# Kernel tuning notes

Hardware: AMD Instinct MI355X
Metric: run time of the kernel (lower is better)

## Reference

```python
import jax, jax.numpy as jnp
import numpy as np

NU, NBU, NI, D, L = 50000, 20000, 100000, 64, 2
C_TEMP = 0.25


def setup_inputs() -> dict:
    key = jax.random.key(0)
    ks = jax.random.split(key, 11)
    B, E_ui, E_ub, E_bi = 2048, 1_500_000, 1_000_000, 1_000_000
    return {
        "users": jax.random.randint(ks[0], (B,), 0, NU, dtype=jnp.int32),
        "bundles": jax.random.randint(ks[1], (B, 2), 0, NBU, dtype=jnp.int32),
        "ui_u": jax.random.randint(ks[2], (E_ui,), 0, NU, dtype=jnp.int32),
        "ui_i": jax.random.randint(ks[3], (E_ui,), 0, NI, dtype=jnp.int32),
        "ub_u": jax.random.randint(ks[4], (E_ub,), 0, NU, dtype=jnp.int32),
        "ub_b": jax.random.randint(ks[5], (E_ub,), 0, NBU, dtype=jnp.int32),
        "bi_b": jax.random.randint(ks[6], (E_bi,), 0, NBU, dtype=jnp.int32),
        "bi_i": jax.random.randint(ks[7], (E_bi,), 0, NI, dtype=jnp.int32),
        "users_feature": jax.random.normal(ks[8], (NU, D), jnp.float32) * 0.1,
        "bundles_feature": jax.random.normal(ks[9], (NBU, D), jnp.float32) * 0.1,
        "items_feature": jax.random.normal(ks[10], (NI, D), jnp.float32) * 0.1,
    }


def _sym_norm_vals(rows, cols, n):
    # laplace_transform: D_r^{-1/2} A D_c^{-1/2}; graph is symmetric so row/col degrees coincide
    deg = jax.ops.segment_sum(jnp.ones(rows.shape, jnp.float32), rows, num_segments=n)
    dinv = 1.0 / (jnp.sqrt(deg) + 1e-8)
    return dinv[rows] * dinv[cols]


def _spmm(rows, cols, vals, feat, n):
    return jax.ops.segment_sum(vals[:, None] * feat[cols], rows, num_segments=n)


def _one_propagate(rows, cols, n, A, Bf):
    vals = _sym_norm_vals(rows, cols, n)
    f = jnp.concatenate([A, Bf], axis=0)  # [n, D]
    acc = f
    for i in range(L):
        f = _spmm(rows, cols, vals, f, n) / (i + 2)
        nrm = jnp.maximum(jnp.linalg.norm(f, axis=1, keepdims=True), 1e-12)
        acc = acc + f / nrm  # sum of L2-normalized layer outputs + layer0
    return acc[: A.shape[0]], acc[A.shape[0]:]


def _bundle_agg(bi_b, bi_i, il_items):
    # row-normalized bundle-item aggregation: diag(1/bundle_size) @ BI
    deg = jax.ops.segment_sum(jnp.ones(bi_b.shape, jnp.float32), bi_b, num_segments=NBU)
    w = (1.0 / (deg + 1e-8))[bi_b]
    return jax.ops.segment_sum(w[:, None] * il_items[bi_i], bi_b, num_segments=NBU)


def _c_loss(pos, aug):
    pos = pos[:, 0, :]
    aug = aug[:, 0, :]
    pos = pos / jnp.maximum(jnp.linalg.norm(pos, axis=1, keepdims=True), 1e-12)
    aug = aug / jnp.maximum(jnp.linalg.norm(aug, axis=1, keepdims=True), 1e-12)
    pos_score = jnp.sum(pos * aug, axis=1) / C_TEMP
    ttl = jnp.matmul(pos, aug.T) / C_TEMP  # [B, B]
    return -jnp.mean(pos_score - jax.nn.logsumexp(ttl, axis=1))


def reference(users, bundles, ui_u, ui_i, ub_u, ub_b, bi_b, bi_i,
              users_feature, bundles_feature, items_feature):
    # item-level graph: [[0, UI], [UI^T, 0]], size NU+NI (symmetric directed edge list)
    il_rows = jnp.concatenate([ui_u, ui_i + NU])
    il_cols = jnp.concatenate([ui_i + NU, ui_u])
    IL_users, IL_items = _one_propagate(il_rows, il_cols, NU + NI, users_feature, items_feature)
    IL_bundles = _bundle_agg(bi_b, bi_i, IL_items)

    # bundle-level graph: [[0, UB], [UB^T, 0]], size NU+NBU
    bl_rows = jnp.concatenate([ub_u, ub_b + NU])
    bl_cols = jnp.concatenate([ub_b + NU, ub_u])
    BL_users, BL_bundles = _one_propagate(bl_rows, bl_cols, NU + NBU, users_feature, bundles_feature)

    nb = bundles.shape[1]
    IL_u = jnp.broadcast_to(IL_users[users][:, None, :], (users.shape[0], nb, D))
    BL_u = jnp.broadcast_to(BL_users[users][:, None, :], (users.shape[0], nb, D))
    IL_b = IL_bundles[bundles]  # [B, nb, D]
    BL_b = BL_bundles[bundles]

    pred = jnp.sum(IL_u * IL_b, axis=2) + jnp.sum(BL_u * BL_b, axis=2)  # [B, 2]
    bpr_loss = -jnp.mean(jax.nn.log_sigmoid(pred[:, 0:1] - pred[:, 1:2]))

    c_loss = 0.5 * (_c_loss(IL_u, BL_u) + _c_loss(IL_b, BL_b))
    return jnp.stack([bpr_loss, c_loss])


if __name__ == "__main__":
    out = reference(**setup_inputs())
    print(out)
```

## Files before the change

### kernel.cpp

```cpp
#include <hip/hip_runtime.h>
#include <hip/hip_bf16.h>
#include <math.h>

static constexpr int NUc  = 50000;
static constexpr int NBUc = 20000;
static constexpr int NIc  = 100000;
static constexpr int NILc = 150000;
static constexpr int NBLc = 70000;
static constexpr int GUB0   = 150016;
static constexpr int GBI0   = 220032;
static constexpr int BK_UB0 = 1172;
static constexpr int BK_BI0 = 1719;
static constexpr int NBK    = 1876;
static constexpr int GTOT   = NBK * 128;
static constexpr float SCL  = 64.0f;
typedef float floatx2 __attribute__((ext_vector_type(2)));

__device__ __forceinline__ float wredsum(float v) {
  #pragma unroll
  for (int m = 32; m >= 1; m >>= 1) v += __shfl_xor(v, m, 64);
  return v;
}
__device__ __forceinline__ float bf2f(unsigned short h) {
  return __uint_as_float(((unsigned int)h) << 16);
}
__device__ __forceinline__ unsigned short f2bf(float f) {
  unsigned int u = __float_as_uint(f);
  return (unsigned short)((u + 0x7FFFu + ((u >> 16) & 1u)) >> 16);
}
__device__ __forceinline__ float fp8_1(unsigned int w, int byteIdx) {
  return __builtin_amdgcn_cvt_f32_fp8((w >> (8 * byteIdx)) & 0xFFu, 0);
}

__global__ void k_bcount_all(const int* __restrict__ ui_u, const int* __restrict__ ui_i,
                             const int* __restrict__ ub_u, const int* __restrict__ ub_b,
                             const int* __restrict__ bi_b,
                             int E_ui, int E_ub, int E_bi, int* __restrict__ bCnt) {
  __shared__ int hist[NBK];
  for (int i = threadIdx.x; i < NBK; i += 256) hist[i] = 0;
  __syncthreads();
  int b = blockIdx.x;
  if (b < 512) {
    int chunk = (E_ui + 511) / 512, c0 = b * chunk, c1 = min(E_ui, c0 + chunk);
    for (int e = c0 + (int)threadIdx.x; e < c1; e += 256) {
      atomicAdd(&hist[ui_u[e] >> 7], 1);
      atomicAdd(&hist[(ui_i[e] + NUc) >> 7], 1);
    }
  } else if (b < 768) {
    int lb = b - 512, chunk = (E_ub + 255) / 256, c0 = lb * chunk, c1 = min(E_ub, c0 + chunk);
    for (int e = c0 + (int)threadIdx.x; e < c1; e += 256) {
      atomicAdd(&hist[(GUB0 + ub_u[e]) >> 7], 1);
      atomicAdd(&hist[(GUB0 + NUc + ub_b[e]) >> 7], 1);
    }
  } else {
    int lb = b - 768, chunk = (E_bi + 255) / 256, c0 = lb * chunk, c1 = min(E_bi, c0 + chunk);
    for (int e = c0 + (int)threadIdx.x; e < c1; e += 256)
      atomicAdd(&hist[(GBI0 + bi_b[e]) >> 7], 1);
  }
  __syncthreads();
  for (int i = threadIdx.x; i < NBK; i += 256)
    if (hist[i]) atomicAdd(&bCnt[i], hist[i]);
}

__global__ void k_scan2048(const int* __restrict__ in, int n,
                           int* __restrict__ outBase, int* __restrict__ outCur) {
  __shared__ int sh[512];
  int t = threadIdx.x, i0 = 4 * t;
  int v0 = (i0 < n) ? in[i0] : 0;
  int v1 = (i0 + 1 < n) ? in[i0 + 1] : 0;
  int v2 = (i0 + 2 < n) ? in[i0 + 2] : 0;
  int v3 = (i0 + 3 < n) ? in[i0 + 3] : 0;
  int ts = v0 + v1 + v2 + v3;
  sh[t] = ts;
  __syncthreads();
  for (int o = 1; o < 512; o <<= 1) {
    int x = (t >= o) ? sh[t - o] : 0;
    __syncthreads();
    sh[t] += x;
    __syncthreads();
  }
  int ex = sh[t] - ts;
  if (i0 < n)     { outBase[i0] = ex;                    outCur[i0] = ex; }
  if (i0 + 1 < n) { outBase[i0 + 1] = ex + v0;           outCur[i0 + 1] = ex + v0; }
  if (i0 + 2 < n) { outBase[i0 + 2] = ex + v0 + v1;      outCur[i0 + 2] = ex + v0 + v1; }
  if (i0 + 3 < n) { outBase[i0 + 3] = ex + v0 + v1 + v2; outCur[i0 + 3] = ex + v0 + v1 + v2; }
  if (t == 511) outBase[n] = sh[511];
}

__global__ void k_bin_all(const int* __restrict__ ui_u, const int* __restrict__ ui_i,
                          const int* __restrict__ ub_u, const int* __restrict__ ub_b,
                          const int* __restrict__ bi_b, const int* __restrict__ bi_i,
                          int E_ui, int E_ub, int E_bi,
                          int* __restrict__ bCur, unsigned int* __restrict__ binned) {
  __shared__ int hist[NBK];
  __shared__ int base[NBK];
  for (int i = threadIdx.x; i < NBK; i += 256) hist[i] = 0;
  __syncthreads();
  int b = blockIdx.x;
  int c0, c1, seg;
  if (b < 512)      { seg = 0; int ch = (E_ui + 511) / 512; c0 = b * ch; c1 = min(E_ui, c0 + ch); }
  else if (b < 768) { seg = 1; int ch = (E_ub + 255) / 256; c0 = (b - 512) * ch; c1 = min(E_ub, c0 + ch); }
  else              { seg = 2; int ch = (E_bi + 255) / 256; c0 = (b - 768) * ch; c1 = min(E_bi, c0 + ch); }
  for (int e = c0 + (int)threadIdx.x; e < c1; e += 256) {
    if (seg == 0) {
      atomicAdd(&hist[ui_u[e] >> 7], 1);
      atomicAdd(&hist[(ui_i[e] + NUc) >> 7], 1);
    } else if (seg == 1) {
      atomicAdd(&hist[(GUB0 + ub_u[e]) >> 7], 1);
      atomicAdd(&hist[(GUB0 + NUc + ub_b[e]) >> 7], 1);
    } else {
      atomicAdd(&hist[(GBI0 + bi_b[e]) >> 7], 1);
    }
  }
  __syncthreads();
  for (int i = threadIdx.x; i < NBK; i += 256) {
    int h = hist[i];
    base[i] = h ? atomicAdd(&bCur[i], h) : 0;
    hist[i] = 0;
  }
  __syncthreads();
  for (int e = c0 + (int)threadIdx.x; e < c1; e += 256) {
    if (seg == 0) {
      int u = ui_u[e], x = ui_i[e] + NUc;
      int b1 = u >> 7;
      binned[base[b1] + atomicAdd(&hist[b1], 1)] = ((unsigned)(u & 127) << 18) | (unsigned)x;
      int b2 = x >> 7;
      binned[base[b2] + atomicAdd(&hist[b2], 1)] = ((unsigned)(x & 127) << 18) | (unsigned)u;
    } else if (seg == 1) {
      int ul = ub_u[e], bl = NUc + ub_b[e];
      int r1 = GUB0 + ul, r2 = GUB0 + bl;
      int b1 = r1 >> 7;
      binned[base[b1] + atomicAdd(&hist[b1], 1)] = ((unsigned)(r1 & 127) << 18) | (unsigned)bl;
      int b2 = r2 >> 7;
      binned[base[b2] + atomicAdd(&hist[b2], 1)] = ((unsigned)(r2 & 127) << 18) | (unsigned)ul;
    } else {
      int r = GBI0 + bi_b[e];
      int b1 = r >> 7;
      binned[base[b1] + atomicAdd(&hist[b1], 1)] = ((unsigned)(r & 127) << 18) | (unsigned)bi_i[e];
    }
  }
}

__global__ void k_rowhist_all(const unsigned int* __restrict__ binned, const int* __restrict__ bBase,
                              int* __restrict__ cnt) {
  __shared__ int hist[128];
  int bk = blockIdx.x, rowbase = bk << 7;
  int s = bBase[bk], e = bBase[bk + 1];
  if (threadIdx.x < 128) hist[threadIdx.x] = 0;
  __syncthreads();
  for (int i = s + (int)threadIdx.x; i < e; i += 256)
    atomicAdd(&hist[binned[i] >> 18], 1);
  __syncthreads();
  if (threadIdx.x < 128) cnt[rowbase + (int)threadIdx.x] = hist[threadIdx.x];
}

__global__ void k_scan_block_pad(const int* __restrict__ in, int n, int* __restrict__ out,
                                 int* __restrict__ bsum) {
  __shared__ int sh[256];
  int t = threadIdx.x;
  long base = (long)blockIdx.x * 1024 + (long)t * 4;
  int v0 = (base     < n) ? ((in[base]     + 15) & ~15) : 0;
  int v1 = (base + 1 < n) ? ((in[base + 1] + 15) & ~15) : 0;
  int v2 = (base + 2 < n) ? ((in[base + 2] + 15) & ~15) : 0;
  int v3 = (base + 3 < n) ? ((in[base + 3] + 15) & ~15) : 0;
  int tsum = v0 + v1 + v2 + v3;
  sh[t] = tsum;
  __syncthreads();
  for (int o = 1; o < 256; o <<= 1) {
    int x = (t >= o) ? sh[t - o] : 0;
    __syncthreads();
    sh[t] += x;
    __syncthreads();
  }
  int excl = sh[t] - tsum;
  if (t == 255) bsum[blockIdx.x] = sh[255];
  if (base     < n) out[base]     = excl;
  if (base + 1 < n) out[base + 1] = excl + v0;
  if (base + 2 < n) out[base + 2] = excl + v0 + v1;
  if (base + 3 < n) out[base + 3] = excl + v0 + v1 + v2;
}

__global__ void k_scan_bsum(int* __restrict__ bsum, int nb) {
  __shared__ int sh[256];
  int t = threadIdx.x;
  int v = (t < nb) ? bsum[t] : 0;
  sh[t] = v;
  __syncthreads();
  for (int o = 1; o < 256; o <<= 1) {
    int x = (t >= o) ? sh[t - o] : 0;
    __syncthreads();
    sh[t] += x;
    __syncthreads();
  }
  if (t < nb) bsum[t] = sh[t] - v;
}

__global__ void k_scan_add(int* __restrict__ out, int n, const int* __restrict__ bsum) {
  long i = (long)blockIdx.x * 256 + threadIdx.x;
  if (i < n) out[i] += bsum[i >> 10];
}

__global__ void k_csrfill_all(const unsigned int* __restrict__ binned, const int* __restrict__ bBase,
                              const int* __restrict__ rp, int* __restrict__ colv) {
  __shared__ int cur[128];
  int bk = blockIdx.x, rowbase = bk << 7;
  int xb, zpad;
  if (bk < BK_UB0)      { xb = 0;    zpad = NILc; }
  else if (bk < BK_BI0) { xb = GUB0; zpad = GUB0 + NBLc; }
  else                  { xb = 0;    zpad = NIc; }
  int s = bBase[bk], e = bBase[bk + 1];
  if (threadIdx.x < 128) cur[threadIdx.x] = rp[rowbase + (int)threadIdx.x];
  __syncthreads();
  for (int i = s + (int)threadIdx.x; i < e; i += 256) {
    unsigned int pk = binned[i];
    int pos = atomicAdd(&cur[pk >> 18], 1);
    colv[pos] = xb + (int)(pk & 0x3FFFFu);
  }
  __syncthreads();
  if (threadIdx.x < 128) {
    int r = rowbase + (int)threadIdx.x;
    int end = rp[r + 1];
    for (int k = cur[threadIdx.x]; k < end; k++) colv[k] = zpad;
  }
}

__global__ void k_prescale_all(const int* __restrict__ cnt, const float* __restrict__ userF,
                               const float* __restrict__ bundF, const float* __restrict__ itemF,
                               unsigned int* __restrict__ X) {
  long idx = (long)blockIdx.x * 256 + threadIdx.x;
  if (idx >= (long)GBI0 * 16) return;
  int g = (int)(idx >> 4), k4 = ((int)idx & 15) << 2;
  float4 v = make_float4(0.f, 0.f, 0.f, 0.f);
  if (g < NILc) {
    const float* src = (g < NUc) ? userF + (long)g * 64 : itemF + (long)(g - NUc) * 64;
    v = *(const float4*)(src + k4);
  } else if (g >= GUB0 && g < GUB0 + NBLc) {
    int l = g - GUB0;
    const float* src = (l < NUc) ? userF + (long)l * 64 : bundF + (long)(l - NUc) * 64;
    v = *(const float4*)(src + k4);
  }
  float f = SCL / (sqrtf((float)cnt[g]) + 1e-8f);
  unsigned int w = 0;
  w = __builtin_amdgcn_cvt_pk_fp8_f32(v.x * f, v.y * f, w, false);
  w = __builtin_amdgcn_cvt_pk_fp8_f32(v.z * f, v.w * f, w, true);
  X[idx] = w;
}

__global__ void k_spmm_g(const int* __restrict__ rp, const int* __restrict__ cnt,
                         const int* __restrict__ col, const unsigned int* __restrict__ X,
                         unsigned int* __restrict__ outF8, unsigned short* __restrict__ outB16,
                         float* __restrict__ outInv, float scale, int n) {
  int row = blockIdx.x * 4 + (threadIdx.x >> 6);
  if (row >= n) return;
  int lane = threadIdx.x & 63, q = lane >> 4, p = lane & 15;
  int s = rp[row], e = rp[row + 1];
  const unsigned int* Xp = X + p;
  float a0 = 0.f, a1 = 0.f, a2 = 0.f, a3 = 0.f;
  for (int eo = s + q; eo < e; eo += 16) {
    int c0 = col[eo], c1 = col[eo + 4], c2 = col[eo + 8], c3 = col[eo + 12];
    unsigned int w0 = Xp[(size_t)c0 << 4];
    unsigned int w1 = Xp[(size_t)c1 << 4];
    unsigned int w2 = Xp[(size_t)c2 << 4];
    unsigned int w3 = Xp[(size_t)c3 << 4];
    floatx2 l0 = __builtin_amdgcn_cvt_pk_f32_fp8(w0, false);
    floatx2 h0 = __builtin_amdgcn_cvt_pk_f32_fp8(w0, true);
    floatx2 l1 = __builtin_amdgcn_cvt_pk_f32_fp8(w1, false);
    floatx2 h1 = __builtin_amdgcn_cvt_pk_f32_fp8(w1, true);
    floatx2 l2 = __builtin_amdgcn_cvt_pk_f32_fp8(w2, false);
    floatx2 h2 = __builtin_amdgcn_cvt_pk_f32_fp8(w2, true);
    floatx2 l3 = __builtin_amdgcn_cvt_pk_f32_fp8(w3, false);
    floatx2 h3 = __builtin_amdgcn_cvt_pk_f32_fp8(w3, true);
    a0 += (l0.x + l1.x) + (l2.x + l3.x);
    a1 += (l0.y + l1.y) + (l2.y + l3.y);
    a2 += (h0.x + h1.x) + (h2.x + h3.x);
    a3 += (h0.y + h1.y) + (h2.y + h3.y);
  }
  a0 += __shfl_xor(a0, 32, 64); a1 += __shfl_xor(a1, 32, 64);
  a2 += __shfl_xor(a2, 32, 64); a3 += __shfl_xor(a3, 32, 64);
  a0 += __shfl_xor(a0, 16, 64); a1 += __shfl_xor(a1, 16, 64);
  a2 += __shfl_xor(a2, 16, 64); a3 += __shfl_xor(a3, 16, 64);
  float dinv = 1.0f / (sqrtf((float)cnt[row]) + 1e-8f);
  float f = dinv * scale * (1.0f / SCL);
  float r0 = a0 * f, r1 = a1 * f, r2 = a2 * f, r3 = a3 * f;
  float ss = r0 * r0 + r1 * r1 + r2 * r2 + r3 * r3;
  ss += __shfl_xor(ss, 8, 64); ss += __shfl_xor(ss, 4, 64);
  ss += __shfl_xor(ss, 2, 64); ss += __shfl_xor(ss, 1, 64);
  if (q == 0) {
    if (outF8) {
      float mf = dinv * SCL;
      unsigned int w = 0;
      w = __builtin_amdgcn_cvt_pk_fp8_f32(r0 * mf, r1 * mf, w, false);
      w = __builtin_amdgcn_cvt_pk_fp8_f32(r2 * mf, r3 * mf, w, true);
      outF8[(size_t)row * 16 + p] = w;
    } else {
      uint2 m;
      m.x = (unsigned int)f2bf(r0) | ((unsigned int)f2bf(r1) << 16);
      m.y = (unsigned int)f2bf(r2) | ((unsigned int)f2bf(r3) << 16);
      *(uint2*)(outB16 + (size_t)row * 64 + p * 4) = m;
    }
    if (p == 0) outInv[row] = 1.0f / fmaxf(sqrtf(ss), 1e-12f);
  }
}

__global__ void k_agg_g(const int* __restrict__ rp, const int* __restrict__ cnt,
                        const int* __restrict__ col, const unsigned short* __restrict__ MACC,
                        float* __restrict__ ILB, int n) {
  int rl = blockIdx.x * 4 + (threadIdx.x >> 6);
  if (rl >= n) return;
  int row = GBI0 + rl;
  int lane = threadIdx.x & 63, q = lane >> 4, p = lane & 15;
  int s = rp[row], e = rp[row + 1];
  const uint2* Xp = (const uint2*)MACC + p;
  float a0 = 0.f, a1 = 0.f, a2 = 0.f, a3 = 0.f;
  for (int eo = s + q; eo < e; eo += 16) {
    int c0 = col[eo], c1 = col[eo + 4], c2 = col[eo + 8], c3 = col[eo + 12];
    uint2 v0 = Xp[(size_t)c0 << 4];
    uint2 v1 = Xp[(size_t)c1 << 4];
    uint2 v2 = Xp[(size_t)c2 << 4];
    uint2 v3 = Xp[(size_t)c3 << 4];
    a0 += (__uint_as_float(v0.x << 16) + __uint_as_float(v1.x << 16)) +
          (__uint_as_float(v2.x << 16) + __uint_as_float(v3.x << 16));
    a1 += (__uint_as_float(v0.x) + __uint_as_float(v1.x)) +
          (__uint_as_float(v2.x) + __uint_as_float(v3.x));
    a2 += (__uint_as_float(v0.y << 16) + __uint_as_float(v1.y << 16)) +
          (__uint_as_float(v2.y << 16) + __uint_as_float(v3.y << 16));
    a3 += (__uint_as_float(v0.y) + __uint_as_float(v1.y)) +
          (__uint_as_float(v2.y) + __uint_as_float(v3.y));
  }
  a0 += __shfl_xor(a0, 32, 64); a1 += __shfl_xor(a1, 32, 64);
  a2 += __shfl_xor(a2, 32, 64); a3 += __shfl_xor(a3, 32, 64);
  a0 += __shfl_xor(a0, 16, 64); a1 += __shfl_xor(a1, 16, 64);
  a2 += __shfl_xor(a2, 16, 64); a3 += __shfl_xor(a3, 16, 64);
  if (q == 0) {
    float w = 1.0f / ((float)cnt[row] + 1e-8f);
    *(float4*)(ILB + (size_t)rl * 64 + p * 4) = make_float4(a0 * w, a1 * w, a2 * w, a3 * w);
  }
}

__global__ void k_acc_items(const float* __restrict__ itemF, const int* __restrict__ cnt,
                            const unsigned int* __restrict__ M1, const unsigned short* __restrict__ F2b,
                            const float* __restrict__ INV1, const float* __restrict__ INV2,
                            unsigned short* __restrict__ MACC) {
  long idx = (long)blockIdx.x * 256 + threadIdx.x;
  if (idx >= (long)NIc * 64) return;
  int rl = (int)(idx >> 6), d = (int)(idx & 63);
  int g = NUc + rl;
  long gi = (long)g * 64 + d;
  float rs = sqrtf((float)cnt[g]) + 1e-8f;
  float m1v = fp8_1(M1[gi >> 2], d & 3) * (1.0f / SCL);
  float res = itemF[idx] + m1v * rs * INV1[g] + bf2f(F2b[gi]) * INV2[g];
  MACC[idx] = f2bf(res);
}

__global__ void k_batch(const int* __restrict__ users, const int* __restrict__ bundles,
                        const float* __restrict__ userF, const float* __restrict__ bundF,
                        const int* __restrict__ cnt,
                        const unsigned int* __restrict__ M1, const unsigned short* __restrict__ F2b,
                        const float* __restrict__ INV1, const float* __restrict__ INV2,
                        const float* __restrict__ ILB, int B,
                        float* __restrict__ ILu, float* __restrict__ BLu,
                        float* __restrict__ ILb2, float* __restrict__ BLb2,
                        float* __restrict__ PN1, float* __restrict__ AN1,
                        float* __restrict__ PN2, float* __restrict__ AN2) {
  int w = blockIdx.x * 4 + (threadIdx.x >> 6);
  int lane = threadIdx.x & 63;
  if (w >= 6 * B) return;
  float val;
  float* rawDst; float* nrmDst = nullptr; int nrmRow = 0;
  if (w < 2 * B) {
    bool il = w < B;
    int j = il ? w : w - B;
    int u = users[j];
    int g = il ? u : GUB0 + u;
    long gi = (long)g * 64 + lane;
    float rs = sqrtf((float)cnt[g]) + 1e-8f;
    float m1v = fp8_1(M1[gi >> 2], lane & 3) * (1.0f / SCL);
    val = userF[(long)u * 64 + lane] + m1v * rs * INV1[g] + bf2f(F2b[gi]) * INV2[g];
    rawDst = (il ? ILu : BLu) + (long)j * 64;
    nrmDst = il ? PN1 : AN1; nrmRow = j;
  } else if (w < 4 * B) {
    int j = w - 2 * B;
    int b = bundles[j];
    val = ILB[(long)b * 64 + lane];
    rawDst = ILb2 + (long)j * 64;
    if ((j & 1) == 0) { nrmDst = PN2; nrmRow = j >> 1; }
  } else {
    int j = w - 4 * B;
    int b = bundles[j];
    int g = GUB0 + NUc + b;
    long gi = (long)g * 64 + lane;
    float rs = sqrtf((float)cnt[g]) + 1e-8f;
    float m1v = fp8_1(M1[gi >> 2], lane & 3) * (1.0f / SCL);
    val = bundF[(long)b * 64 + lane] + m1v * rs * INV1[g] + bf2f(F2b[gi]) * INV2[g];
    rawDst = BLb2 + (long)j * 64;
    if ((j & 1) == 0) { nrmDst = AN2; nrmRow = j >> 1; }
  }
  rawDst[lane] = val;
  float ss = wredsum(val * val);
  if (nrmDst) nrmDst[(long)nrmRow * 64 + lane] = val * (1.0f / fmaxf(sqrtf(ss), 1e-12f));
}

__global__ void k_bpr(const float* __restrict__ ILu, const float* __restrict__ ILb2,
                      const float* __restrict__ BLu, const float* __restrict__ BLb2,
                      int B, float* __restrict__ out) {
  int row = blockIdx.x * 4 + (threadIdx.x >> 6);
  int lane = threadIdx.x & 63;
  if (row >= B) return;
  float t = ILu[(long)row * 64 + lane] *
              (ILb2[(long)(2 * row) * 64 + lane] - ILb2[(long)(2 * row + 1) * 64 + lane]) +
            BLu[(long)row * 64 + lane] *
              (BLb2[(long)(2 * row) * 64 + lane] - BLb2[(long)(2 * row + 1) * 64 + lane]);
  float x = wredsum(t);
  if (lane == 0) {
    float ls = -(fmaxf(-x, 0.0f) + log1pf(expf(-fabsf(x))));
    unsafeAtomicAdd(&out[0], -ls / (float)B);
  }
}

__global__ void k_gemm_lse(const float* __restrict__ P1, const float* __restrict__ A1,
                           const float* __restrict__ P2, const float* __restrict__ A2,
                           float* __restrict__ Pm, float* __restrict__ Ps,
                           float* __restrict__ Diag, int N, float scale) {
  __shared__ float PsS[64][129];
  __shared__ float AsS[64][129];
  constexpr float L2E = 1.44269504f;
  const float* P = blockIdx.z ? P2 : P1;
  const float* A = blockIdx.z ? A2 : A1;
  int bi0 = blockIdx.y * 128, bj0 = blockIdx.x * 128;
  int t = threadIdx.x;
  #pragma unroll
  for (int sct = 0; sct < 8; sct++) {
    int idx4 = t + sct * 256;
    int r = idx4 >> 4, k = (idx4 & 15) << 2;
    int pr = min(bi0 + r, N - 1);
    int ar = min(bj0 + r, N - 1);
    float4 v = *(const float4*)(P + (long)pr * 64 + k);
    PsS[k][r] = v.x; PsS[k + 1][r] = v.y; PsS[k + 2][r] = v.z; PsS[k + 3][r] = v.w;
    float4 w = *(const float4*)(A + (long)ar * 64 + k);
    AsS[k][r] = w.x; AsS[k + 1][r] = w.y; AsS[k + 2][r] = w.z; AsS[k + 3][r] = w.w;
  }
  __syncthreads();
  int tx = t & 15, ty = t >> 4;
  float acc[8][8];
  #pragma unroll
  for (int i = 0; i < 8; i++)
    #pragma unroll
    for (int j = 0; j < 8; j++) acc[i][j] = 0.0f;
  #pragma unroll 4
  for (int k = 0; k < 64; k++) {
    float a[8], b[8];
    #pragma unroll
    for (int i = 0; i < 8; i++) a[i] = PsS[k][ty * 8 + i];
    #pragma unroll
    for (int j = 0; j < 8; j++) b[j] = AsS[k][tx + 16 * j];
    #pragma unroll
    for (int i = 0; i < 8; i++)
      #pragma unroll
      for (int j = 0; j < 8; j++) acc[i][j] = fmaf(a[i], b[j], acc[i][j]);
  }
  bool diagBlk = (blockIdx.x == blockIdx.y);
  #pragma unroll
  for (int i = 0; i < 8; i++) {
    int lrow = ty * 8 + i;
    float xs[8], tm = -1e30f;
    #pragma unroll
    for (int j = 0; j < 8; j++) { xs[j] = acc[i][j] * scale; tm = fmaxf(tm, xs[j]); }
    float tsum = 0.f;
    #pragma unroll
    for (int j = 0; j < 8; j++) tsum += exp2f((xs[j] - tm) * L2E);
    #pragma unroll
    for (int o = 1; o <= 8; o <<= 1) {
      float m2 = __shfl_xor(tm, o, 64), s2 = __shfl_xor(tsum, o, 64);
      float M = fmaxf(tm, m2);
      tsum = tsum * exp2f((tm - M) * L2E) + s2 * exp2f((m2 - M) * L2E);
      tm = M;
    }
    if (tx == 0) {
      size_t o = ((size_t)blockIdx.z * N + bi0 + lrow) * 16 + blockIdx.x;
      Pm[o] = tm; Ps[o] = tsum;
    }
    if (diagBlk && tx == (lrow & 15))
      Diag[(size_t)blockIdx.z * N + bi0 + lrow] = xs[lrow >> 4];
  }
}

__global__ void k_lse_final(const float* __restrict__ Pm, const float* __restrict__ Ps,
                            const float* __restrict__ Diag, int N, float coeff,
                            float* __restrict__ out) {
  constexpr float L2E = 1.44269504f;
  int idx = blockIdx.x * 4 + (threadIdx.x >> 6);
  if (idx >= 2 * N) return;
  int z = idx >= N ? 1 : 0, r = idx - z * N;
  int lane = threadIdx.x & 63;
  float m = -1e30f, s = 0.f;
  if (lane < 16) {
    size_t o = ((size_t)z * N + r) * 16 + lane;
    m = Pm[o]; s = Ps[o];
  }
  #pragma unroll
  for (int o = 8; o >= 1; o >>= 1) {
    float m2 = __shfl_xor(m, o, 64), s2 = __shfl_xor(s, o, 64);
    float M = fmaxf(m, m2);
    s = s * exp2f((m - M) * L2E) + s2 * exp2f((m2 - M) * L2E);
    m = M;
  }
  if (lane == 0) {
    float lse = m + log2f(s) * 0.69314718f;
    unsafeAtomicAdd(&out[1], -(Diag[(size_t)z * N + r] - lse) * coeff);
  }
}

extern "C" void kernel_launch(void* const* d_in, const int* in_sizes, int n_in,
                              void* d_out, int out_size, void* d_ws, size_t ws_size,
                              hipStream_t stream) {
  const int* users   = (const int*)d_in[0];
  const int* bundles = (const int*)d_in[1];
  const int* ui_u    = (const int*)d_in[2];
  const int* ui_i    = (const int*)d_in[3];
  const int* ub_u    = (const int*)d_in[4];
  const int* ub_b    = (const int*)d_in[5];
  const int* bi_b    = (const int*)d_in[6];
  const int* bi_i    = (const int*)d_in[7];
  const float* userF = (const float*)d_in[8];
  const float* bundF = (const float*)d_in[9];
  const float* itemF = (const float*)d_in[10];
  float* out = (float*)d_out;

  const int B    = in_sizes[0];
  const int E_ui = in_sizes[2];
  const int E_ub = in_sizes[4];
  const int E_bi = in_sizes[6];
  const long E_all = 2L * E_ui + 2L * E_ub + E_bi;

  float* ws = (float*)d_ws;
  size_t off = 0;
  auto alloc = [&](size_t nfloat) -> float* {
    float* p = ws + off;
    off += (nfloat + 63) & ~(size_t)63;
    return p;
  };
  unsigned int* X  = (unsigned int*)alloc((size_t)GBI0 * 16);
  unsigned int* M1 = (unsigned int*)alloc((size_t)GBI0 * 16);
  unsigned short* F2b = (unsigned short*)alloc((size_t)GBI0 * 32);
  unsigned int* binned = (unsigned int*)alloc((size_t)E_all);
  int* colv  = (int*)alloc((size_t)E_all + 15 * (size_t)GTOT + 128);
  int* rp    = (int*)alloc(GTOT + 1);
  int* cnt   = (int*)alloc(GTOT + 1);
  float* INV1 = alloc(GTOT);
  float* INV2 = alloc(GTOT);
  float* ILB  = alloc((size_t)NBUc * 64);
  float* ILu  = alloc((size_t)B * 64);
  float* BLu  = alloc((size_t)B * 64);
  float* ILb2 = alloc((size_t)B * 128);
  float* BLb2 = alloc((size_t)B * 128);
  float* PN1  = alloc((size_t)B * 64);
  float* AN1  = alloc((size_t)B * 64);
  float* PN2  = alloc((size_t)B * 64);
  float* AN2  = alloc((size_t)B * 64);
  float* Pm   = alloc((size_t)2 * B * 16);
  float* Ps   = alloc((size_t)2 * B * 16);
  float* Diag = alloc((size_t)2 * B);
  int* bCnt  = (int*)alloc(2049);
  int* bBase = (int*)alloc(2049);
  int* bCur  = (int*)alloc(2049);
  int* bsum  = (int*)alloc(256);
  (void)ws_size; (void)n_in; (void)out_size;

  unsigned short* MACC = (unsigned short*)binned;

  hipMemsetAsync(bCnt, 0, sizeof(int) * NBK, stream);
  k_bcount_all<<<1024, 256, 0, stream>>>(ui_u, ui_i, ub_u, ub_b, bi_b, E_ui, E_ub, E_bi, bCnt);
  k_scan2048<<<1, 512, 0, stream>>>(bCnt, NBK, bBase, bCur);
  k_bin_all<<<1024, 256, 0, stream>>>(ui_u, ui_i, ub_u, ub_b, bi_b, bi_i,
                                      E_ui, E_ub, E_bi, bCur, binned);
  hipMemsetAsync(cnt, 0, sizeof(int) * (GTOT + 1), stream);
  k_rowhist_all<<<NBK, 256, 0, stream>>>(binned, bBase, cnt);
  {
    int scan_n = GTOT + 1;
    int nb1 = (scan_n + 1023) / 1024;
    k_scan_block_pad<<<nb1, 256, 0, stream>>>(cnt, scan_n, rp, bsum);
    k_scan_bsum<<<1, 256, 0, stream>>>(bsum, nb1);
    k_scan_add<<<(scan_n + 255) / 256, 256, 0, stream>>>(rp, scan_n, bsum);
  }
  k_csrfill_all<<<NBK, 256, 0, stream>>>(binned, bBase, rp, colv);

  k_prescale_all<<<(int)(((long)GBI0 * 16 + 255) / 256), 256, 0, stream>>>(cnt, userF, bundF,
                                                                           itemF, X);
  k_spmm_g<<<(GBI0 + 3) / 4, 256, 0, stream>>>(rp, cnt, colv, X, M1, nullptr, INV1, 0.5f, GBI0);
  k_spmm_g<<<(GBI0 + 3) / 4, 256, 0, stream>>>(rp, cnt, colv, M1, nullptr, F2b, INV2,
                                               1.0f / 3.0f, GBI0);
  hipMemsetAsync(MACC + (size_t)NIc * 64, 0, 128, stream);
  k_acc_items<<<(int)(((long)NIc * 64 + 255) / 256), 256, 0, stream>>>(
      itemF, cnt, M1, F2b, INV1, INV2, MACC);
  k_agg_g<<<(NBUc + 3) / 4, 256, 0, stream>>>(rp, cnt, colv, MACC, ILB, NBUc);
  k_batch<<<(6 * B + 3) / 4, 256, 0, stream>>>(users, bundles, userF, bundF, cnt, M1, F2b,
                                               INV1, INV2, ILB, B,
                                               ILu, BLu, ILb2, BLb2, PN1, AN1, PN2, AN2);

  hipMemsetAsync(out, 0, 2 * sizeof(float), stream);
  k_bpr<<<(B + 3) / 4, 256, 0, stream>>>(ILu, ILb2, BLu, BLb2, B, out);
  dim3 gg((B + 127) / 128, (B + 127) / 128, 2);
  k_gemm_lse<<<gg, 256, 0, stream>>>(PN1, AN1, PN2, AN2, Pm, Ps, Diag, B, 4.0f);
  k_lse_final<<<(2 * B + 3) / 4, 256, 0, stream>>>(Pm, Ps, Diag, B, 0.5f / (float)B, out);
}
```

Before: 492.4 us.

## Fuse item accumulation into second SpMM and aggregate only batch bundles

The second SpMM pass now directly forms the final item-level embedding (input features plus both normalized layers) and writes it as FP8, removing the separate k_acc_items pass and its bf16 intermediate. Bundle aggregation is run only for the 2*B bundles referenced by the batch instead of all 20000 bundles, and it writes the gathered and normalized outputs directly, so k_batch shrinks. Item rows no longer store F2b/INV2, and storing the accumulated item features in FP8 adds quantization error to the bundle embeddings.

```diff
diff --git a/kernel.cpp b/kernel.cpp
--- a/kernel.cpp
+++ b/kernel.cpp
@@ -249,7 +249,10 @@
 __global__ void k_spmm_g(const int* __restrict__ rp, const int* __restrict__ cnt,
                          const int* __restrict__ col, const unsigned int* __restrict__ X,
                          unsigned int* __restrict__ outF8, unsigned short* __restrict__ outB16,
-                         float* __restrict__ outInv, float scale, int n) {
+                         float* __restrict__ outInv,
+                         const float* __restrict__ itemF, const float* __restrict__ INV1in,
+                         unsigned int* __restrict__ MACC8,
+                         float scale, int n) {
   int row = blockIdx.x * 4 + (threadIdx.x >> 6);
   if (row >= n) return;
   int lane = threadIdx.x & 63, q = lane >> 4, p = lane & 15;
@@ -279,77 +282,94 @@
   a2 += __shfl_xor(a2, 32, 64); a3 += __shfl_xor(a3, 32, 64);
   a0 += __shfl_xor(a0, 16, 64); a1 += __shfl_xor(a1, 16, 64);
   a2 += __shfl_xor(a2, 16, 64); a3 += __shfl_xor(a3, 16, 64);
-  float dinv = 1.0f / (sqrtf((float)cnt[row]) + 1e-8f);
+  float rs = sqrtf((float)cnt[row]) + 1e-8f;
+  float dinv = 1.0f / rs;
   float f = dinv * scale * (1.0f / SCL);
   float r0 = a0 * f, r1 = a1 * f, r2 = a2 * f, r3 = a3 * f;
   float ss = r0 * r0 + r1 * r1 + r2 * r2 + r3 * r3;
   ss += __shfl_xor(ss, 8, 64); ss += __shfl_xor(ss, 4, 64);
   ss += __shfl_xor(ss, 2, 64); ss += __shfl_xor(ss, 1, 64);
-  if (q == 0) {
-    if (outF8) {
-      float mf = dinv * SCL;
-      unsigned int w = 0;
-      w = __builtin_amdgcn_cvt_pk_fp8_f32(r0 * mf, r1 * mf, w, false);
-      w = __builtin_amdgcn_cvt_pk_fp8_f32(r2 * mf, r3 * mf, w, true);
-      outF8[(size_t)row * 16 + p] = w;
-    } else {
-      uint2 m;
-      m.x = (unsigned int)f2bf(r0) | ((unsigned int)f2bf(r1) << 16);
-      m.y = (unsigned int)f2bf(r2) | ((unsigned int)f2bf(r3) << 16);
-      *(uint2*)(outB16 + (size_t)row * 64 + p * 4) = m;
-    }
+  if (q != 0) return;
+  if (outF8) {
+    float mf = dinv * SCL;
+    unsigned int w = 0;
+    w = __builtin_amdgcn_cvt_pk_fp8_f32(r0 * mf, r1 * mf, w, false);
+    w = __builtin_amdgcn_cvt_pk_fp8_f32(r2 * mf, r3 * mf, w, true);
+    outF8[(size_t)row * 16 + p] = w;
     if (p == 0) outInv[row] = 1.0f / fmaxf(sqrtf(ss), 1e-12f);
-  }
-}
-
-__global__ void k_agg_g(const int* __restrict__ rp, const int* __restrict__ cnt,
-                        const int* __restrict__ col, const unsigned short* __restrict__ MACC,
-                        float* __restrict__ ILB, int n) {
-  int rl = blockIdx.x * 4 + (threadIdx.x >> 6);
-  if (rl >= n) return;
-  int row = GBI0 + rl;
+    return;
+  }
+  if (row >= NUc && row < NILc) {
+    float inv2 = 1.0f / fmaxf(sqrtf(ss), 1e-12f);
+    unsigned int m1w = Xp[(size_t)row << 4];
+    floatx2 mlo = __builtin_amdgcn_cvt_pk_f32_fp8(m1w, false);
+    floatx2 mhi = __builtin_amdgcn_cvt_pk_f32_fp8(m1w, true);
+    float s1 = rs * INV1in[row] * (1.0f / SCL);
+    float4 bf = *(const float4*)(itemF + (long)(row - NUc) * 64 + p * 4);
+    float o0 = bf.x + mlo.x * s1 + r0 * inv2;
+    float o1 = bf.y + mlo.y * s1 + r1 * inv2;
+    float o2 = bf.z + mhi.x * s1 + r2 * inv2;
+    float o3 = bf.w + mhi.y * s1 + r3 * inv2;
+    unsigned int w = 0;
+    w = __builtin_amdgcn_cvt_pk_fp8_f32(o0 * SCL, o1 * SCL, w, false);
+    w = __builtin_amdgcn_cvt_pk_fp8_f32(o2 * SCL, o3 * SCL, w, true);
+    MACC8[(size_t)(row - NUc) * 16 + p] = w;
+  } else {
+    uint2 m;
+    m.x = (unsigned int)f2bf(r0) | ((unsigned int)f2bf(r1) << 16);
+    m.y = (unsigned int)f2bf(r2) | ((unsigned int)f2bf(r3) << 16);
+    *(uint2*)(outB16 + (size_t)row * 64 + p * 4) = m;
+    if (p == 0) outInv[row] = 1.0f / fmaxf(sqrtf(ss), 1e-12f);
+  }
+}
+
+__global__ void k_agg_batch(const int* __restrict__ rp, const int* __restrict__ cnt,
+                            const int* __restrict__ col, const unsigned int* __restrict__ MACC8,
+                            const int* __restrict__ bundles, int nb2,
+                            float* __restrict__ ILb2, float* __restrict__ PN2) {
+  int j = blockIdx.x * 4 + (threadIdx.x >> 6);
+  if (j >= nb2) return;
+  int row = GBI0 + bundles[j];
   int lane = threadIdx.x & 63, q = lane >> 4, p = lane & 15;
   int s = rp[row], e = rp[row + 1];
-  const uint2* Xp = (const uint2*)MACC + p;
+  const unsigned int* Xp = MACC8 + p;
   float a0 = 0.f, a1 = 0.f, a2 = 0.f, a3 = 0.f;
   for (int eo = s + q; eo < e; eo += 16) {
     int c0 = col[eo], c1 = col[eo + 4], c2 = col[eo + 8], c3 = col[eo + 12];
-    uint2 v0 = Xp[(size_t)c0 << 4];
-    uint2 v1 = Xp[(size_t)c1 << 4];
-    uint2 v2 = Xp[(size_t)c2 << 4];
-    uint2 v3 = Xp[(size_t)c3 << 4];
-    a0 += (__uint_as_float(v0.x << 16) + __uint_as_float(v1.x << 16)) +
-          (__uint_as_float(v2.x << 16) + __uint_as_float(v3.x << 16));
-    a1 += (__uint_as_float(v0.x) + __uint_as_float(v1.x)) +
-          (__uint_as_float(v2.x) + __uint_as_float(v3.x));
-    a2 += (__uint_as_float(v0.y << 16) + __uint_as_float(v1.y << 16)) +
-          (__uint_as_float(v2.y << 16) + __uint_as_float(v3.y << 16));
-    a3 += (__uint_as_float(v0.y) + __uint_as_float(v1.y)) +
-          (__uint_as_float(v2.y) + __uint_as_float(v3.y));
+    unsigned int w0 = Xp[(size_t)c0 << 4];
+    unsigned int w1 = Xp[(size_t)c1 << 4];
+    unsigned int w2 = Xp[(size_t)c2 << 4];
+    unsigned int w3 = Xp[(size_t)c3 << 4];
+    floatx2 l0 = __builtin_amdgcn_cvt_pk_f32_fp8(w0, false);
+    floatx2 h0 = __builtin_amdgcn_cvt_pk_f32_fp8(w0, true);
+    floatx2 l1 = __builtin_amdgcn_cvt_pk_f32_fp8(w1, false);
+    floatx2 h1 = __builtin_amdgcn_cvt_pk_f32_fp8(w1, true);
+    floatx2 l2 = __builtin_amdgcn_cvt_pk_f32_fp8(w2, false);
+    floatx2 h2 = __builtin_amdgcn_cvt_pk_f32_fp8(w2, true);
+    floatx2 l3 = __builtin_amdgcn_cvt_pk_f32_fp8(w3, false);
+    floatx2 h3 = __builtin_amdgcn_cvt_pk_f32_fp8(w3, true);
+    a0 += (l0.x + l1.x) + (l2.x + l3.x);
+    a1 += (l0.y + l1.y) + (l2.y + l3.y);
+    a2 += (h0.x + h1.x) + (h2.x + h3.x);
+    a3 += (h0.y + h1.y) + (h2.y + h3.y);
   }
   a0 += __shfl_xor(a0, 32, 64); a1 += __shfl_xor(a1, 32, 64);
   a2 += __shfl_xor(a2, 32, 64); a3 += __shfl_xor(a3, 32, 64);
   a0 += __shfl_xor(a0, 16, 64); a1 += __shfl_xor(a1, 16, 64);
   a2 += __shfl_xor(a2, 16, 64); a3 += __shfl_xor(a3, 16, 64);
+  float w = (1.0f / SCL) / ((float)cnt[row] + 1e-8f);
+  float r0 = a0 * w, r1 = a1 * w, r2 = a2 * w, r3 = a3 * w;
+  float ss = r0 * r0 + r1 * r1 + r2 * r2 + r3 * r3;
+  ss += __shfl_xor(ss, 8, 64); ss += __shfl_xor(ss, 4, 64);
+  ss += __shfl_xor(ss, 2, 64); ss += __shfl_xor(ss, 1, 64);
   if (q == 0) {
-    float w = 1.0f / ((float)cnt[row] + 1e-8f);
-    *(float4*)(ILB + (size_t)rl * 64 + p * 4) = make_float4(a0 * w, a1 * w, a2 * w, a3 * w);
-  }
-}
-
-__global__ void k_acc_items(const float* __restrict__ itemF, const int* __restrict__ cnt,
-                            const unsigned int* __restrict__ M1, const unsigned short* __restrict__ F2b,
-                            const float* __restrict__ INV1, const float* __restrict__ INV2,
-                            unsigned short* __restrict__ MACC) {
-  long idx = (long)blockIdx.x * 256 + threadIdx.x;
-  if (idx >= (long)NIc * 64) return;
-  int rl = (int)(idx >> 6), d = (int)(idx & 63);
-  int g = NUc + rl;
-  long gi = (long)g * 64 + d;
-  float rs = sqrtf((float)cnt[g]) + 1e-8f;
-  float m1v = fp8_1(M1[gi >> 2], d & 3) * (1.0f / SCL);
-  float res = itemF[idx] + m1v * rs * INV1[g] + bf2f(F2b[gi]) * INV2[g];
-  MACC[idx] = f2bf(res);
+    *(float4*)(ILb2 + (size_t)j * 64 + p * 4) = make_float4(r0, r1, r2, r3);
+    if ((j & 1) == 0) {
+      float inv = 1.0f / fmaxf(sqrtf(ss), 1e-12f);
+      *(float4*)(PN2 + (size_t)(j >> 1) * 64 + p * 4) =
+          make_float4(r0 * inv, r1 * inv, r2 * inv, r3 * inv);
+    }
+  }
 }
 
 __global__ void k_batch(const int* __restrict__ users, const int* __restrict__ bundles,
@@ -357,14 +377,14 @@
                         const int* __restrict__ cnt,
                         const unsigned int* __restrict__ M1, const unsigned short* __restrict__ F2b,
                         const float* __restrict__ INV1, const float* __restrict__ INV2,
-                        const float* __restrict__ ILB, int B,
+                        int B,
                         float* __restrict__ ILu, float* __restrict__ BLu,
-                        float* __restrict__ ILb2, float* __restrict__ BLb2,
+                        float* __restrict__ BLb2,
                         float* __restrict__ PN1, float* __restrict__ AN1,
-                        float* __restrict__ PN2, float* __restrict__ AN2) {
+                        float* __restrict__ AN2) {
   int w = blockIdx.x * 4 + (threadIdx.x >> 6);
   int lane = threadIdx.x & 63;
-  if (w >= 6 * B) return;
+  if (w >= 4 * B) return;
   float val;
   float* rawDst; float* nrmDst = nullptr; int nrmRow = 0;
   if (w < 2 * B) {
@@ -378,14 +398,8 @@
     val = userF[(long)u * 64 + lane] + m1v * rs * INV1[g] + bf2f(F2b[gi]) * INV2[g];
     rawDst = (il ? ILu : BLu) + (long)j * 64;
     nrmDst = il ? PN1 : AN1; nrmRow = j;
-  } else if (w < 4 * B) {
+  } else {
     int j = w - 2 * B;
-    int b = bundles[j];
-    val = ILB[(long)b * 64 + lane];
-    rawDst = ILb2 + (long)j * 64;
-    if ((j & 1) == 0) { nrmDst = PN2; nrmRow = j >> 1; }
-  } else {
-    int j = w - 4 * B;
     int b = bundles[j];
     int g = GUB0 + NUc + b;
     long gi = (long)g * 64 + lane;
@@ -548,7 +562,6 @@
   int* cnt   = (int*)alloc(GTOT + 1);
   float* INV1 = alloc(GTOT);
   float* INV2 = alloc(GTOT);
-  float* ILB  = alloc((size_t)NBUc * 64);
   float* ILu  = alloc((size_t)B * 64);
   float* BLu  = alloc((size_t)B * 64);
   float* ILb2 = alloc((size_t)B * 128);
@@ -566,7 +579,7 @@
   int* bsum  = (int*)alloc(256);
   (void)ws_size; (void)n_in; (void)out_size;
 
-  unsigned short* MACC = (unsigned short*)binned;
+  unsigned int* MACC8 = (unsigned int*)binned;
 
   hipMemsetAsync(bCnt, 0, sizeof(int) * NBK, stream);
   k_bcount_all<<<1024, 256, 0, stream>>>(ui_u, ui_i, ub_u, ub_b, bi_b, E_ui, E_ub, E_bi, bCnt);
@@ -586,16 +599,15 @@
 
   k_prescale_all<<<(int)(((long)GBI0 * 16 + 255) / 256), 256, 0, stream>>>(cnt, userF, bundF,
                                                                            itemF, X);
-  k_spmm_g<<<(GBI0 + 3) / 4, 256, 0, stream>>>(rp, cnt, colv, X, M1, nullptr, INV1, 0.5f, GBI0);
+  k_spmm_g<<<(GBI0 + 3) / 4, 256, 0, stream>>>(rp, cnt, colv, X, M1, nullptr, INV1,
+                                               nullptr, nullptr, nullptr, 0.5f, GBI0);
+  hipMemsetAsync(MACC8 + (size_t)NIc * 16, 0, 64, stream);
   k_spmm_g<<<(GBI0 + 3) / 4, 256, 0, stream>>>(rp, cnt, colv, M1, nullptr, F2b, INV2,
-                                               1.0f / 3.0f, GBI0);
-  hipMemsetAsync(MACC + (size_t)NIc * 64, 0, 128, stream);
-  k_acc_items<<<(int)(((long)NIc * 64 + 255) / 256), 256, 0, stream>>>(
-      itemF, cnt, M1, F2b, INV1, INV2, MACC);
-  k_agg_g<<<(NBUc + 3) / 4, 256, 0, stream>>>(rp, cnt, colv, MACC, ILB, NBUc);
-  k_batch<<<(6 * B + 3) / 4, 256, 0, stream>>>(users, bundles, userF, bundF, cnt, M1, F2b,
-                                               INV1, INV2, ILB, B,
-                                               ILu, BLu, ILb2, BLb2, PN1, AN1, PN2, AN2);
+                                               itemF, INV1, MACC8, 1.0f / 3.0f, GBI0);
+  k_agg_batch<<<(2 * B + 3) / 4, 256, 0, stream>>>(rp, cnt, colv, MACC8, bundles, 2 * B,
+                                                   ILb2, PN2);
+  k_batch<<<(4 * B + 3) / 4, 256, 0, stream>>>(users, bundles, userF, bundF, cnt, M1, F2b,
+                                               INV1, INV2, B, ILu, BLu, BLb2, PN1, AN1, AN2);
 
   hipMemsetAsync(out, 0, 2 * sizeof(float), stream);
   k_bpr<<<(B + 3) / 4, 256, 0, stream>>>(ILu, ILb2, BLu, BLb2, B, out);
```

Result: faster. 472.3 us (-4.1%).
